# Performance work log

Measured on AMD Instinct MI355X. Metric: run time of the kernel, lower is better.

## Reference

```python
import jax, jax.numpy as jnp
import numpy as np

N_NODES = 50000
N_EDGES = 400000
N_GRAPHS = 16
IN_DIM_NODE = 6
IN_DIM_EDGE = 2
HIDDEN = 64
N_LAYERS = 3
STATE_DIM = 4
MLP1, MLP2 = 256, 256
MAX_ACTION = 1.0
BN_EPS = 1e-5


def _lin(key, fan_in, fan_out):
    k1, k2 = jax.random.split(key)
    s = 1.0 / np.sqrt(fan_in)
    w = jax.random.uniform(k1, (fan_in, fan_out), minval=-s, maxval=s, dtype=jnp.float32)
    b = jax.random.uniform(k2, (fan_out,), minval=-s, maxval=s, dtype=jnp.float32)
    return w, b


def setup_inputs() -> dict:
    key = jax.random.key(0)
    ks = jax.random.split(key, 32)
    inp = {}
    inp["state"] = jax.random.normal(ks[0], (N_GRAPHS, STATE_DIM), dtype=jnp.float32)
    inp["h_feat"] = jax.random.normal(ks[1], (N_NODES, IN_DIM_NODE), dtype=jnp.float32)
    # positive edge features (distances) bounded away from 0 since forward takes 1/e
    inp["e_feat"] = jax.random.uniform(ks[2], (N_EDGES, IN_DIM_EDGE), minval=0.5, maxval=1.5, dtype=jnp.float32)
    inp["src"] = jax.random.randint(ks[3], (N_EDGES,), 0, N_NODES, dtype=jnp.int32)
    inp["dst"] = jax.random.randint(ks[4], (N_EDGES,), 0, N_NODES, dtype=jnp.int32)
    inp["graph_ids"] = jnp.sort(jax.random.randint(ks[5], (N_NODES,), 0, N_GRAPHS, dtype=jnp.int32))
    inp["emb_h_w"], inp["emb_h_b"] = _lin(ks[6], IN_DIM_NODE, HIDDEN)
    inp["emb_e_w"], inp["emb_e_b"] = _lin(ks[7], IN_DIM_EDGE, HIDDEN)
    for i, name in enumerate(["A", "B", "C", "D", "E"]):
        ws, bs = [], []
        for l in range(N_LAYERS):
            w, b = _lin(jax.random.fold_in(ks[8 + i], l), HIDDEN, HIDDEN)
            ws.append(w); bs.append(b)
        inp[name + "_w"] = jnp.stack(ws)  # [L, H, H]
        inp[name + "_b"] = jnp.stack(bs)  # [L, H]
    inp["bn_h_g"] = jnp.ones((N_LAYERS, HIDDEN), jnp.float32)
    inp["bn_h_b"] = jnp.zeros((N_LAYERS, HIDDEN), jnp.float32)
    inp["bn_e_g"] = jnp.ones((N_LAYERS, HIDDEN), jnp.float32)
    inp["bn_e_b"] = jnp.zeros((N_LAYERS, HIDDEN), jnp.float32)
    inp["l1_w"], inp["l1_b"] = _lin(ks[13], HIDDEN + STATE_DIM, MLP1)
    inp["l2_w"], inp["l2_b"] = _lin(ks[14], MLP1, MLP2)
    inp["l3_w"], inp["l3_b"] = _lin(ks[15], MLP2, 2)
    return inp


def _bn(x, g, b):
    mu = jnp.mean(x, axis=0)
    var = jnp.var(x, axis=0)
    return (x - mu) * jax.lax.rsqrt(var + BN_EPS) * g + b


def reference(state, h_feat, e_feat, src, dst, graph_ids,
              emb_h_w, emb_h_b, emb_e_w, emb_e_b,
              A_w, A_b, B_w, B_b, C_w, C_b, D_w, D_b, E_w, E_b,
              bn_h_g, bn_h_b, bn_e_g, bn_e_b,
              l1_w, l1_b, l2_w, l2_b, l3_w, l3_b):
    N = h_feat.shape[0]
    B = state.shape[0]
    # feature prep: concat node states, reciprocal edge states
    e = 1.0 / e_feat
    h = h_feat @ emb_h_w + emb_h_b          # [N, H]
    e = e @ emb_e_w + emb_e_b               # [E, H]
    for l in range(N_LAYERS):
        h_in, e_in = h, e
        Ah = h @ A_w[l] + A_b[l]
        Bh = h @ B_w[l] + B_b[l]
        Dh = h @ D_w[l] + D_b[l]
        Eh = h @ E_w[l] + E_b[l]
        Ce = e @ C_w[l] + C_b[l]
        e_hat = Dh[src] + Eh[dst] + Ce      # [E, H] edge gates pre-activation
        sigma = jax.nn.sigmoid(e_hat)
        num = jax.ops.segment_sum(sigma * Bh[src], dst, num_segments=N)
        den = jax.ops.segment_sum(sigma, dst, num_segments=N)
        h_new = Ah + num / (den + 1e-6)
        h = h_in + jax.nn.relu(_bn(h_new, bn_h_g[l], bn_h_b[l]))
        e = e_in + jax.nn.relu(_bn(e_hat, bn_e_g[l], bn_e_b[l]))
    # mean readout per graph
    counts = jax.ops.segment_sum(jnp.ones((N,), h.dtype), graph_ids, num_segments=B)
    hg = jax.ops.segment_sum(h, graph_ids, num_segments=B) / counts[:, None]
    x = jnp.concatenate([hg, state], axis=-1)
    x = jax.nn.relu(x @ l1_w + l1_b)
    x = jax.nn.relu(x @ l2_w + l2_b)
    return MAX_ACTION * jnp.tanh(x @ l3_w + l3_b)
```

## Files before the change

kernel.cpp:

```cpp
#include <hip/hip_runtime.h>
#include <hip/hip_fp16.h>
#include <math.h>
#include <string.h>

#define NN 50000
#define NE 400000

__device__ __forceinline__ void atomAddF(float* p, float v) { unsafeAtomicAdd(p, v); }
__device__ __forceinline__ double atomAddD(double* p, double v) { return unsafeAtomicAdd(p, v); }
__device__ __forceinline__ int atomAddI(int* p, int v) { return atomicAdd(p, v); }

typedef _Float16 h2v __attribute__((ext_vector_type(2)));

__device__ __forceinline__ float2 up2h(unsigned v) {
  __half2 h; memcpy(&h, &v, 4); return __half22float2(h);
}
__device__ __forceinline__ unsigned pk2h(float a, float b) {
  __half2 h = __floats2half2_rn(a, b);
  unsigned v; memcpy(&v, &h, 4); return v;
}
__device__ __forceinline__ void up8(uint4 u, float* f) {
  float2 a = up2h(u.x), b = up2h(u.y), c = up2h(u.z), d = up2h(u.w);
  f[0] = a.x; f[1] = a.y; f[2] = b.x; f[3] = b.y;
  f[4] = c.x; f[5] = c.y; f[6] = d.x; f[7] = d.y;
}
__device__ __forceinline__ uint4 pk8(const float* f) {
  uint4 u;
  u.x = pk2h(f[0], f[1]); u.y = pk2h(f[2], f[3]);
  u.z = pk2h(f[4], f[5]); u.w = pk2h(f[6], f[7]);
  return u;
}

#if __has_builtin(__builtin_amdgcn_fdot2)
__device__ __forceinline__ float dot2(unsigned a, unsigned b, float c) {
  return __builtin_amdgcn_fdot2(__builtin_bit_cast(h2v, a), __builtin_bit_cast(h2v, b), c, false);
}
#else
__device__ __forceinline__ float dot2(unsigned a, unsigned b, float c) {
  float2 fa = up2h(a), fb = up2h(b);
  return c + fa.x * fb.x + fa.y * fb.y;
}
#endif

#define SW(kk) ((((kk) & 7)) << 2)

__global__ __launch_bounds__(256) void k_zero(float4* __restrict__ p, int n4) {
  int i = blockIdx.x * 256 + threadIdx.x;
  int s = gridDim.x * 256;
  for (; i < n4; i += s) p[i] = make_float4(0.f, 0.f, 0.f, 0.f);
}

__global__ __launch_bounds__(256) void k_deg(const int* __restrict__ dst, int* __restrict__ deg) {
  int i = blockIdx.x * 256 + threadIdx.x;
  if (i < NE) atomAddI(&deg[dst[i]], 1);
}

__global__ __launch_bounds__(1024) void k_scan(int* __restrict__ degcur,
    int* __restrict__ offs, double* __restrict__ stats) {
  __shared__ int wsum[16];
  int t = threadIdx.x;
  int lane = t & 63, w = t >> 6;
  if (t < 256) stats[t] = 0.0;
  int carry = 0;
  for (int base = 0; base < NN; base += 1024) {
    int i = base + t;
    int v = (i < NN) ? degcur[i] : 0;
    int x = v;
    #pragma unroll
    for (int off = 1; off < 64; off <<= 1) {
      int y = __shfl_up(x, off);
      if (lane >= off) x += y;
    }
    if (lane == 63) wsum[w] = x;
    __syncthreads();
    if (w == 0 && lane < 16) {
      int s = wsum[lane];
      #pragma unroll
      for (int off = 1; off < 16; off <<= 1) {
        int y = __shfl_up(s, off);
        if (lane >= off) s += y;
      }
      wsum[lane] = s;
    }
    __syncthreads();
    int wbase = (w > 0) ? wsum[w - 1] : 0;
    int total = wsum[15];
    int excl = carry + wbase + x - v;
    if (i < NN) { offs[i] = excl; degcur[i] = excl; }
    carry += total;
    __syncthreads();
  }
  if (t == 0) offs[NN] = carry;
}

__global__ __launch_bounds__(256) void k_scatter(const int* __restrict__ dst,
    const int* __restrict__ src, const float* __restrict__ e_feat,
    int* __restrict__ cursor,
    int* __restrict__ srcp, int* __restrict__ dstp, float* __restrict__ ef2) {
  int i = blockIdx.x * 256 + threadIdx.x;
  if (i < NE) {
    int d = dst[i];
    int p = atomAddI(&cursor[d], 1);
    srcp[p] = src[i];
    dstp[p] = d;
    ((float2*)ef2)[p] = ((const float2*)e_feat)[i];
  }
}

template <int MODE>
__global__ __launch_bounds__(512) void k_node_gemm(float* __restrict__ h,
    const __half* __restrict__ Ah_in, const float* __restrict__ bnp,
    const float* __restrict__ hf, const float* __restrict__ ehw,
    const float* __restrict__ ehb,
    const float* __restrict__ w0, const float* __restrict__ w1,
    const float* __restrict__ w2, const float* __restrict__ w3,
    const float* __restrict__ b0, const float* __restrict__ b1,
    const float* __restrict__ b2, const float* __restrict__ b3,
    __half* __restrict__ Ah16, __half* __restrict__ Bh16,
    __half* __restrict__ Dh16, __half* __restrict__ Eh16) {
  __shared__ __align__(16) unsigned hsU[32 * 256];
  __shared__ __align__(16) unsigned wshU[32 * 64];
  int t = threadIdx.x;
  int n0 = blockIdx.x * 256;
  #pragma unroll
  for (int i = 0; i < 8; ++i) {
    int f = (t + i * 512) * 4;
    int r = f >> 6;
    int k = f & 63;
    int n = n0 + r;
    float4 v = make_float4(0.f, 0.f, 0.f, 0.f);
    if (n < NN) {
      size_t idx = (size_t)n * 64 + k;
      if (MODE == 2) {
        const float* row = hf + (size_t)n * 6;
        v = *(const float4*)(ehb + k);
        #pragma unroll
        for (int q = 0; q < 6; ++q) {
          float x = row[q];
          float4 wv = *(const float4*)(ehw + q * 64 + k);
          v.x += x * wv.x; v.y += x * wv.y; v.z += x * wv.z; v.w += x * wv.w;
        }
        *(float4*)(h + idx) = v;
      } else {
        v = *(const float4*)(h + idx);
        if (MODE == 1) {
          uint2 au = *(const uint2*)(Ah_in + idx);
          float2 a01 = up2h(au.x), a23 = up2h(au.y);
          float4 sc4 = *(const float4*)(bnp + k);
          float4 sh4 = *(const float4*)(bnp + 64 + k);
          v.x += fmaxf(a01.x * sc4.x + sh4.x, 0.f);
          v.y += fmaxf(a01.y * sc4.y + sh4.y, 0.f);
          v.z += fmaxf(a23.x * sc4.z + sh4.z, 0.f);
          v.w += fmaxf(a23.y * sc4.w + sh4.w, 0.f);
          *(float4*)(h + idx) = v;
        }
      }
    }
    int kk0 = k >> 1;
    hsU[(kk0 + 0) * 256 + (r ^ SW(kk0 + 0))] = pk2h(v.x, v.y);
    hsU[(kk0 + 1) * 256 + (r ^ SW(kk0 + 1))] = pk2h(v.z, v.w);
  }
  int cg = t & 7, rg = t >> 3;
  int cb = cg * 8;
  #pragma unroll 1
  for (int y = 0; y < 4; ++y) {
    const float* W = (y == 0) ? w0 : (y == 1) ? w1 : (y == 2) ? w2 : w3;
    const float* B = (y == 0) ? b0 : (y == 1) ? b1 : (y == 2) ? b2 : b3;
    __syncthreads();
    #pragma unroll
    for (int i = 0; i < 4; ++i) {
      int idx = t + i * 512;
      int kk = idx >> 6, j = idx & 63;
      wshU[idx] = pk2h(W[(2 * kk) * 64 + j], W[(2 * kk + 1) * 64 + j]);
    }
    __syncthreads();
    float acc[4][8];
    #pragma unroll
    for (int r = 0; r < 4; ++r)
      #pragma unroll
      for (int j = 0; j < 8; ++j) acc[r][j] = 0.f;
    #pragma unroll 8
    for (int kk = 0; kk < 32; ++kk) {
      uint4 a4 = *(const uint4*)&hsU[kk * 256 + ((rg * 4) ^ SW(kk))];
      uint4 wA = *(const uint4*)&wshU[kk * 64 + cb];
      uint4 wB = *(const uint4*)&wshU[kk * 64 + cb + 4];
      unsigned av[4] = {a4.x, a4.y, a4.z, a4.w};
      unsigned wv[8] = {wA.x, wA.y, wA.z, wA.w, wB.x, wB.y, wB.z, wB.w};
      #pragma unroll
      for (int r = 0; r < 4; ++r)
        #pragma unroll
        for (int j = 0; j < 8; ++j) acc[r][j] = dot2(av[r], wv[j], acc[r][j]);
    }
    float4 bv0 = *(const float4*)(B + cb);
    float4 bv1 = *(const float4*)(B + cb + 4);
    float bv[8] = {bv0.x, bv0.y, bv0.z, bv0.w, bv1.x, bv1.y, bv1.z, bv1.w};
    __half* oh = (y == 0) ? Ah16 : (y == 1) ? Bh16 : (y == 2) ? Dh16 : Eh16;
    #pragma unroll
    for (int r = 0; r < 4; ++r) {
      int n = n0 + rg * 4 + r;
      if (n < NN) {
        float o[8];
        #pragma unroll
        for (int j = 0; j < 8; ++j) o[j] = acc[r][j] + bv[j];
        *(uint4*)(oh + (size_t)n * 64 + cb) = pk8(o);
      }
    }
  }
}

template <int MODE, int ESTATS, int EWRITE>
__global__ __launch_bounds__(512) void k_edge_f(__half* __restrict__ e16,
    __half* __restrict__ eh16,
    const float* __restrict__ Cw, const float* __restrict__ Cb,
    const int* __restrict__ srcp, const int* __restrict__ dstp,
    const __half* __restrict__ Dh16, const __half* __restrict__ Eh16,
    const float* __restrict__ bnp, double* __restrict__ stats,
    const float* __restrict__ ef2, const float* __restrict__ ew,
    const float* __restrict__ eb) {
  __shared__ __align__(16) unsigned esU[32 * 256];
  __shared__ __align__(16) unsigned cwU[32 * 64];
  int t = threadIdx.x;
  int e0 = blockIdx.x * 256;
  #pragma unroll
  for (int i = 0; i < 4; ++i) {
    int idx = t + i * 512;
    int kk = idx >> 6, j = idx & 63;
    cwU[idx] = pk2h(Cw[(2 * kk) * 64 + j], Cw[(2 * kk + 1) * 64 + j]);
  }
  #pragma unroll
  for (int i = 0; i < 4; ++i) {
    int f = (t + i * 512) * 8;
    int r = f >> 6;
    int k = f & 63;
    int row = e0 + r;
    uint4 raw = make_uint4(0u, 0u, 0u, 0u);
    if (row < NE) {
      size_t idx = (size_t)row * 64 + k;
      if (MODE == 2) {
        float2 rp = ((const float2*)ef2)[row];
        float r0 = 1.0f / rp.x;
        float r1 = 1.0f / rp.y;
        float4 bA = *(const float4*)(eb + k), bB = *(const float4*)(eb + k + 4);
        float4 waA = *(const float4*)(ew + k), waB = *(const float4*)(ew + k + 4);
        float4 wbA = *(const float4*)(ew + 64 + k), wbB = *(const float4*)(ew + 64 + k + 4);
        float v[8];
        v[0] = bA.x + r0 * waA.x + r1 * wbA.x;
        v[1] = bA.y + r0 * waA.y + r1 * wbA.y;
        v[2] = bA.z + r0 * waA.z + r1 * wbA.z;
        v[3] = bA.w + r0 * waA.w + r1 * wbA.w;
        v[4] = bB.x + r0 * waB.x + r1 * wbB.x;
        v[5] = bB.y + r0 * waB.y + r1 * wbB.y;
        v[6] = bB.z + r0 * waB.z + r1 * wbB.z;
        v[7] = bB.w + r0 * waB.w + r1 * wbB.w;
        raw = pk8(v);
        if (EWRITE) *(uint4*)(e16 + idx) = raw;
      } else {
        raw = *(const uint4*)(e16 + idx);
        if (MODE == 1) {
          float v[8], pp[8];
          up8(raw, v);
          up8(*(const uint4*)(eh16 + idx), pp);
          float4 scA = *(const float4*)(bnp + 128 + k);
          float4 scB = *(const float4*)(bnp + 128 + k + 4);
          float4 shA = *(const float4*)(bnp + 192 + k);
          float4 shB = *(const float4*)(bnp + 192 + k + 4);
          float sc[8] = {scA.x, scA.y, scA.z, scA.w, scB.x, scB.y, scB.z, scB.w};
          float sh[8] = {shA.x, shA.y, shA.z, shA.w, shB.x, shB.y, shB.z, shB.w};
          #pragma unroll
          for (int j = 0; j < 8; ++j) v[j] += fmaxf(pp[j] * sc[j] + sh[j], 0.f);
          raw = pk8(v);
          if (EWRITE) *(uint4*)(e16 + idx) = raw;
        }
      }
    }
    int kk0 = k >> 1;
    esU[(kk0 + 0) * 256 + (r ^ SW(kk0 + 0))] = raw.x;
    esU[(kk0 + 1) * 256 + (r ^ SW(kk0 + 1))] = raw.y;
    esU[(kk0 + 2) * 256 + (r ^ SW(kk0 + 2))] = raw.z;
    esU[(kk0 + 3) * 256 + (r ^ SW(kk0 + 3))] = raw.w;
  }
  __syncthreads();
  int cg = t & 7, rg = t >> 3;
  int cb = cg * 8;
  float acc[4][8];
  #pragma unroll
  for (int r = 0; r < 4; ++r)
    #pragma unroll
    for (int j = 0; j < 8; ++j) acc[r][j] = 0.f;
  #pragma unroll 8
  for (int kk = 0; kk < 32; ++kk) {
    uint4 a4 = *(const uint4*)&esU[kk * 256 + ((rg * 4) ^ SW(kk))];
    uint4 wA = *(const uint4*)&cwU[kk * 64 + cb];
    uint4 wB = *(const uint4*)&cwU[kk * 64 + cb + 4];
    unsigned av[4] = {a4.x, a4.y, a4.z, a4.w};
    unsigned wv[8] = {wA.x, wA.y, wA.z, wA.w, wB.x, wB.y, wB.z, wB.w};
    #pragma unroll
    for (int r = 0; r < 4; ++r)
      #pragma unroll
      for (int j = 0; j < 8; ++j) acc[r][j] = dot2(av[r], wv[j], acc[r][j]);
  }
  float4 cb0 = *(const float4*)(Cb + cb);
  float4 cb1 = *(const float4*)(Cb + cb + 4);
  float cbv[8] = {cb0.x, cb0.y, cb0.z, cb0.w, cb1.x, cb1.y, cb1.z, cb1.w};
  float psum[8], psq[8];
  #pragma unroll
  for (int j = 0; j < 8; ++j) { psum[j] = 0.f; psq[j] = 0.f; }
  #pragma unroll
  for (int r = 0; r < 4; ++r) {
    int p = e0 + rg * 4 + r;
    if (p < NE) {
      int sN = srcp[p], dN = dstp[p];
      float dd[8], qq[8];
      up8(*(const uint4*)(Dh16 + (size_t)sN * 64 + cb), dd);
      up8(*(const uint4*)(Eh16 + (size_t)dN * 64 + cb), qq);
      float ev[8];
      #pragma unroll
      for (int j = 0; j < 8; ++j) {
        float v = acc[r][j] + cbv[j] + dd[j] + qq[j];
        ev[j] = v;
        if (ESTATS) { psum[j] += v; psq[j] += v * v; }
      }
      *(uint4*)(eh16 + (size_t)p * 64 + cb) = pk8(ev);
    }
  }
  if (ESTATS) {
    float* red = (float*)esU;
    __syncthreads();
    #pragma unroll
    for (int j = 0; j < 8; ++j) red[rg * 65 + cb + j] = psum[j];
    __syncthreads();
    if (t < 64) {
      float s = 0.f;
      #pragma unroll
      for (int i = 0; i < 64; ++i) s += red[i * 65 + t];
      atomAddD(stats + 128 + t, (double)s);
    }
    __syncthreads();
    #pragma unroll
    for (int j = 0; j < 8; ++j) red[rg * 65 + cb + j] = psq[j];
    __syncthreads();
    if (t < 64) {
      float q = 0.f;
      #pragma unroll
      for (int i = 0; i < 64; ++i) q += red[i * 65 + t];
      atomAddD(stats + 192 + t, (double)q);
    }
  }
}

template <int LAST>
__global__ __launch_bounds__(1024) void k_agg(const int* __restrict__ offs,
    const int* __restrict__ srcp, const __half* __restrict__ eh16,
    const __half* __restrict__ Bh16, __half* __restrict__ Ah16, double* __restrict__ stats,
    int* __restrict__ ctr,
    const float* __restrict__ hgam, const float* __restrict__ hbet,
    const float* __restrict__ egam, const float* __restrict__ ebet,
    float* __restrict__ bnp, float* __restrict__ hg) {
  int t = threadIdx.x;
  int c = t & 63;
  int g = t >> 6;
  float psum = 0.f, psq = 0.f;
  #pragma unroll 1
  for (int sub = 0; sub < 8; ++sub) {
    int n = blockIdx.x * 128 + g * 8 + sub;
    if (n < NN) {
      int i0 = offs[n], i1 = offs[n + 1];
      float num = 0.f, den = 0.f;
      int i = i0;
      #pragma unroll 1
      for (; i + 3 < i1; i += 4) {
        float x0 = __half2float(eh16[(size_t)(i + 0) * 64 + c]);
        float x1 = __half2float(eh16[(size_t)(i + 1) * 64 + c]);
        float x2 = __half2float(eh16[(size_t)(i + 2) * 64 + c]);
        float x3 = __half2float(eh16[(size_t)(i + 3) * 64 + c]);
        int s0 = srcp[i], s1 = srcp[i + 1], s2 = srcp[i + 2], s3 = srcp[i + 3];
        float b0 = __half2float(Bh16[(size_t)s0 * 64 + c]);
        float b1 = __half2float(Bh16[(size_t)s1 * 64 + c]);
        float b2 = __half2float(Bh16[(size_t)s2 * 64 + c]);
        float b3 = __half2float(Bh16[(size_t)s3 * 64 + c]);
        float g0 = 1.0f / (1.0f + __expf(-x0));
        float g1 = 1.0f / (1.0f + __expf(-x1));
        float g2 = 1.0f / (1.0f + __expf(-x2));
        float g3 = 1.0f / (1.0f + __expf(-x3));
        num += g0 * b0 + g1 * b1 + g2 * b2 + g3 * b3;
        den += g0 + g1 + g2 + g3;
      }
      #pragma unroll 1
      for (; i < i1; ++i) {
        float x0 = __half2float(eh16[(size_t)i * 64 + c]);
        int s0 = srcp[i];
        float b0 = __half2float(Bh16[(size_t)s0 * 64 + c]);
        float g0 = 1.0f / (1.0f + __expf(-x0));
        num += g0 * b0;
        den += g0;
      }
      size_t idx = (size_t)n * 64 + c;
      float v = __half2float(Ah16[idx]) + num / (den + 1e-6f);
      Ah16[idx] = __float2half(v);
      psum += v; psq += v * v;
    }
  }
  __shared__ float red[1024];
  red[t] = psum; __syncthreads();
  if (t < 64) {
    float s = 0.f;
    #pragma unroll
    for (int i = 0; i < 16; ++i) s += red[t + i * 64];
    atomAddD(stats + t, (double)s);
  }
  __syncthreads();
  red[t] = psq; __syncthreads();
  if (t < 64) {
    float q = 0.f;
    #pragma unroll
    for (int i = 0; i < 16; ++i) q += red[t + i * 64];
    atomAddD(stats + 64 + t, (double)q);
  }
  __shared__ int lastFlag;
  __syncthreads();
  if (t == 0) {
    __threadfence();
    int old = atomAddI(ctr, 1);
    lastFlag = (old == (int)gridDim.x - 1);
  }
  __syncthreads();
  if (!lastFlag) return;
  if (t < 64) {
    double s = atomAddD(stats + t, 0.0);
    double q = atomAddD(stats + 64 + t, 0.0);
    double mu = s * (1.0 / NN);
    double var = q * (1.0 / NN) - mu * mu;
    float sc = hgam[t] / sqrtf((float)var + 1e-5f);
    bnp[t] = sc;
    bnp[64 + t] = hbet[t] - (float)mu * sc;
  } else if (t < 128) {
    int cc = t - 64;
    double s = atomAddD(stats + 128 + cc, 0.0);
    double q = atomAddD(stats + 192 + cc, 0.0);
    double mu = s * (1.0 / NE);
    double var = q * (1.0 / NE) - mu * mu;
    float sc = egam[cc] / sqrtf((float)var + 1e-5f);
    bnp[128 + cc] = sc;
    bnp[192 + cc] = ebet[cc] - (float)mu * sc;
  }
  __syncthreads();
  if (t < 256) atomicExch((unsigned long long*)&stats[t], 0ull);
  if (LAST) {
    for (int i = t; i < 1040; i += 1024) hg[i] = 0.f;
  }
}

__global__ __launch_bounds__(256) void k_readout(const float* __restrict__ h,
    const __half* __restrict__ Ah16, const float* __restrict__ bnp,
    const int* __restrict__ gid, float* __restrict__ hg, float* __restrict__ counts) {
  int t = threadIdx.x;
  int c = t & 63;
  int ro = t >> 6;
  int nbase = blockIdx.x * 256;
  float sc = bnp[c], sh = bnp[64 + c];
  float sum = 0.f, cnt = 0.f;
  int curg = -1;
  #pragma unroll 1
  for (int i = 0; i < 64; ++i) {
    int n = nbase + ro + i * 4;
    if (n >= NN) break;
    int g = gid[n];
    if (g != curg) {
      if (curg >= 0) {
        atomAddF(&hg[curg * 64 + c], sum);
        if (c == 0) atomAddF(&counts[curg], cnt);
      }
      curg = g; sum = 0.f; cnt = 0.f;
    }
    size_t idx = (size_t)n * 64 + c;
    float av = __half2float(Ah16[idx]);
    sum += h[idx] + fmaxf(av * sc + sh, 0.f);
    cnt += 1.f;
  }
  if (curg >= 0) {
    atomAddF(&hg[curg * 64 + c], sum);
    if (c == 0) atomAddF(&counts[curg], cnt);
  }
}

__global__ __launch_bounds__(256) void k_mlp(const float* __restrict__ hg, const float* __restrict__ counts,
    const float* __restrict__ state,
    const float* __restrict__ w1, const float* __restrict__ b1,
    const float* __restrict__ w2, const float* __restrict__ b2,
    const float* __restrict__ w3, const float* __restrict__ b3,
    float* __restrict__ out) {
  __shared__ float x0[16][68];
  __shared__ float x1[16][256];
  __shared__ float x2[16][256];
  int t = threadIdx.x;
  for (int idx = t; idx < 16 * 68; idx += 256) {
    int g = idx / 68, c = idx % 68;
    x0[g][c] = (c < 64) ? hg[g * 64 + c] / counts[g] : state[g * 4 + (c - 64)];
  }
  __syncthreads();
  {
    float acc[16];
    float bb = b1[t];
    #pragma unroll
    for (int g = 0; g < 16; ++g) acc[g] = bb;
    for (int k = 0; k < 68; ++k) {
      float w = w1[k * 256 + t];
      #pragma unroll
      for (int g = 0; g < 16; ++g) acc[g] += x0[g][k] * w;
    }
    #pragma unroll
    for (int g = 0; g < 16; ++g) x1[g][t] = fmaxf(acc[g], 0.f);
  }
  __syncthreads();
  {
    float acc[16];
    float bb = b2[t];
    #pragma unroll
    for (int g = 0; g < 16; ++g) acc[g] = bb;
    for (int k = 0; k < 256; ++k) {
      float w = w2[k * 256 + t];
      #pragma unroll
      for (int g = 0; g < 16; ++g) acc[g] += x1[g][k] * w;
    }
    #pragma unroll
    for (int g = 0; g < 16; ++g) x2[g][t] = fmaxf(acc[g], 0.f);
  }
  __syncthreads();
  if (t < 32) {
    int g = t >> 1, o = t & 1;
    float acc = b3[o];
    for (int k = 0; k < 256; ++k) acc += x2[g][k] * w3[k * 2 + o];
    out[g * 2 + o] = tanhf(acc);
  }
}

extern "C" void kernel_launch(void* const* d_in, const int* in_sizes, int n_in,
                              void* d_out, int out_size, void* d_ws, size_t ws_size,
                              hipStream_t stream) {
  const float* state   = (const float*)d_in[0];
  const float* h_feat  = (const float*)d_in[1];
  const float* e_feat  = (const float*)d_in[2];
  const int*   src     = (const int*)d_in[3];
  const int*   dst     = (const int*)d_in[4];
  const int*   gid     = (const int*)d_in[5];
  const float* emb_h_w = (const float*)d_in[6];
  const float* emb_h_b = (const float*)d_in[7];
  const float* emb_e_w = (const float*)d_in[8];
  const float* emb_e_b = (const float*)d_in[9];
  const float* A_w = (const float*)d_in[10];
  const float* A_b = (const float*)d_in[11];
  const float* B_w = (const float*)d_in[12];
  const float* B_b = (const float*)d_in[13];
  const float* C_w = (const float*)d_in[14];
  const float* C_b = (const float*)d_in[15];
  const float* D_w = (const float*)d_in[16];
  const float* D_b = (const float*)d_in[17];
  const float* E_w = (const float*)d_in[18];
  const float* E_b = (const float*)d_in[19];
  const float* bn_h_g = (const float*)d_in[20];
  const float* bn_h_b = (const float*)d_in[21];
  const float* bn_e_g = (const float*)d_in[22];
  const float* bn_e_b = (const float*)d_in[23];
  const float* l1_w = (const float*)d_in[24];
  const float* l1_b = (const float*)d_in[25];
  const float* l2_w = (const float*)d_in[26];
  const float* l2_b = (const float*)d_in[27];
  const float* l3_w = (const float*)d_in[28];
  const float* l3_b = (const float*)d_in[29];

  float* wsp = (float*)d_ws;

  const size_t F_H = (size_t)NN * 64;
  const size_t F_H2 = (size_t)NN * 32;
  const size_t F_E2 = (size_t)NE * 32;
  size_t off = 0;
  float*  h     = wsp + off; off += F_H;
  __half* Ah16  = (__half*)(wsp + off); off += F_H2;
  __half* e16   = (__half*)(wsp + off); off += F_E2;
  __half* eh16  = (__half*)(wsp + off); off += F_E2;
  float*  ef2   = wsp + off; off += (size_t)NE * 2;
  __half* Bh16  = (__half*)(wsp + off); off += F_H2;
  __half* Dh16  = (__half*)(wsp + off); off += F_H2;
  __half* Eh16  = (__half*)(wsp + off); off += F_H2;
  int* srcp    = (int*)(wsp + off); off += NE;
  int* dstp    = (int*)(wsp + off); off += NE;
  int* offs    = (int*)(wsp + off); off += NN + 4;
  int* degcur  = (int*)(wsp + off); off += NN + 4;
  double* stats = (double*)(wsp + off); off += 512;
  float* bnp    = wsp + off; off += 256;
  float* hg     = wsp + off; off += 1024;
  float* counts = hg + 1024; off += 16;
  const size_t need = off * sizeof(float);
  if (ws_size < need) return;
  int* ctr = degcur + NN;

  k_zero<<<64, 256, 0, stream>>>((float4*)degcur, (NN + 4) / 4);
  k_deg<<<(NE + 255) / 256, 256, 0, stream>>>(dst, degcur);
  k_scan<<<1, 1024, 0, stream>>>(degcur, offs, stats);
  k_scatter<<<(NE + 255) / 256, 256, 0, stream>>>(dst, src, e_feat, degcur, srcp, dstp, ef2);

  const int GN = (NN + 255) / 256;
  const int GE = (NE + 255) / 256;
  const int GA = (NN + 127) / 128;
  for (int l = 0; l < 3; ++l) {
    if (l == 0)
      k_node_gemm<2><<<GN, 512, 0, stream>>>(h, Ah16, bnp, h_feat, emb_h_w, emb_h_b,
          A_w, B_w, D_w, E_w, A_b, B_b, D_b, E_b, Ah16, Bh16, Dh16, Eh16);
    else
      k_node_gemm<1><<<GN, 512, 0, stream>>>(h, Ah16, bnp, h_feat, emb_h_w, emb_h_b,
          A_w + l * 4096, B_w + l * 4096, D_w + l * 4096, E_w + l * 4096,
          A_b + l * 64, B_b + l * 64, D_b + l * 64, E_b + l * 64,
          Ah16, Bh16, Dh16, Eh16);
    if (l == 0)
      k_edge_f<2, 1, 1><<<GE, 512, 0, stream>>>(e16, eh16, C_w, C_b,
          srcp, dstp, Dh16, Eh16, bnp, stats, ef2, emb_e_w, emb_e_b);
    else if (l == 1)
      k_edge_f<1, 1, 1><<<GE, 512, 0, stream>>>(e16, eh16, C_w + 4096, C_b + 64,
          srcp, dstp, Dh16, Eh16, bnp, stats, ef2, emb_e_w, emb_e_b);
    else
      k_edge_f<1, 0, 0><<<GE, 512, 0, stream>>>(e16, eh16, C_w + 8192, C_b + 128,
          srcp, dstp, Dh16, Eh16, bnp, stats, ef2, emb_e_w, emb_e_b);
    if (l < 2)
      k_agg<0><<<GA, 1024, 0, stream>>>(offs, srcp, eh16, Bh16, Ah16, stats, ctr + l,
          bn_h_g + l * 64, bn_h_b + l * 64, bn_e_g + l * 64, bn_e_b + l * 64, bnp, hg);
    else
      k_agg<1><<<GA, 1024, 0, stream>>>(offs, srcp, eh16, Bh16, Ah16, stats, ctr + l,
          bn_h_g + l * 64, bn_h_b + l * 64, bn_e_g + l * 64, bn_e_b + l * 64, bnp, hg);
  }
  k_readout<<<(NN + 255) / 256, 256, 0, stream>>>(h, Ah16, bnp, gid, hg, counts);
  k_mlp<<<1, 256, 0, stream>>>(hg, counts, state,
      l1_w, l1_b, l2_w, l2_b, l3_w, l3_b, (float*)d_out);
}
```

Measured before the change: 584.2 us.

## Replace single-block degree scan with three-phase multi-block scan

The exclusive prefix sum over node degrees ran in one 1024-thread block that looped serially over about 49 chunks. It is now split into a per-block local scan, a single-block scan of the 196 block sums, and an add-back pass. This spreads the scan across many CUs, at the cost of two extra kernel launches and an extra intermediate array. The final offset is now written as the constant NE instead of the computed total.

```diff
diff --git a/kernel.cpp b/kernel.cpp
--- a/kernel.cpp
+++ b/kernel.cpp
@@ -55,42 +55,58 @@
   if (i < NE) atomAddI(&deg[dst[i]], 1);
 }
 
-__global__ __launch_bounds__(1024) void k_scan(int* __restrict__ degcur,
-    int* __restrict__ offs, double* __restrict__ stats) {
-  __shared__ int wsum[16];
+__global__ __launch_bounds__(256) void k_scanA(const int* __restrict__ deg,
+    int* __restrict__ locx, int* __restrict__ bsum) {
+  __shared__ int wsum[4];
   int t = threadIdx.x;
+  int i = blockIdx.x * 256 + t;
+  int v = (i < NN) ? deg[i] : 0;
   int lane = t & 63, w = t >> 6;
-  if (t < 256) stats[t] = 0.0;
-  int carry = 0;
-  for (int base = 0; base < NN; base += 1024) {
-    int i = base + t;
-    int v = (i < NN) ? degcur[i] : 0;
-    int x = v;
-    #pragma unroll
-    for (int off = 1; off < 64; off <<= 1) {
-      int y = __shfl_up(x, off);
-      if (lane >= off) x += y;
-    }
-    if (lane == 63) wsum[w] = x;
-    __syncthreads();
-    if (w == 0 && lane < 16) {
-      int s = wsum[lane];
-      #pragma unroll
-      for (int off = 1; off < 16; off <<= 1) {
-        int y = __shfl_up(s, off);
-        if (lane >= off) s += y;
-      }
-      wsum[lane] = s;
-    }
-    __syncthreads();
-    int wbase = (w > 0) ? wsum[w - 1] : 0;
-    int total = wsum[15];
-    int excl = carry + wbase + x - v;
-    if (i < NN) { offs[i] = excl; degcur[i] = excl; }
-    carry += total;
-    __syncthreads();
-  }
-  if (t == 0) offs[NN] = carry;
+  int x = v;
+  #pragma unroll
+  for (int off = 1; off < 64; off <<= 1) {
+    int y = __shfl_up(x, off);
+    if (lane >= off) x += y;
+  }
+  if (lane == 63) wsum[w] = x;
+  __syncthreads();
+  int wbase = 0;
+  #pragma unroll
+  for (int j = 0; j < 4; ++j) if (j < w) wbase += wsum[j];
+  if (i < NN) locx[i] = wbase + x - v;
+  if (t == 255) bsum[blockIdx.x] = wbase + x;
+}
+
+__global__ __launch_bounds__(256) void k_scanB(int* __restrict__ bsum, int nb,
+    double* __restrict__ stats) {
+  __shared__ int wsum[4];
+  int t = threadIdx.x;
+  stats[t] = 0.0;
+  int v = (t < nb) ? bsum[t] : 0;
+  int lane = t & 63, w = t >> 6;
+  int x = v;
+  #pragma unroll
+  for (int off = 1; off < 64; off <<= 1) {
+    int y = __shfl_up(x, off);
+    if (lane >= off) x += y;
+  }
+  if (lane == 63) wsum[w] = x;
+  __syncthreads();
+  int wbase = 0;
+  #pragma unroll
+  for (int j = 0; j < 4; ++j) if (j < w) wbase += wsum[j];
+  if (t < nb) bsum[t] = wbase + x - v;
+}
+
+__global__ __launch_bounds__(256) void k_scanC(const int* __restrict__ locx,
+    const int* __restrict__ bsum, int* __restrict__ offs, int* __restrict__ cursor) {
+  int i = blockIdx.x * 256 + threadIdx.x;
+  if (i < NN) {
+    int v = locx[i] + bsum[blockIdx.x];
+    offs[i] = v;
+    cursor[i] = v;
+  }
+  if (i == 0) offs[NN] = NE;
 }
 
 __global__ __launch_bounds__(256) void k_scatter(const int* __restrict__ dst,
@@ -586,6 +602,8 @@
   int* dstp    = (int*)(wsp + off); off += NE;
   int* offs    = (int*)(wsp + off); off += NN + 4;
   int* degcur  = (int*)(wsp + off); off += NN + 4;
+  int* locx    = (int*)(wsp + off); off += NN;
+  int* bsum    = (int*)(wsp + off); off += 256;
   double* stats = (double*)(wsp + off); off += 512;
   float* bnp    = wsp + off; off += 256;
   float* hg     = wsp + off; off += 1024;
@@ -594,9 +612,13 @@
   if (ws_size < need) return;
   int* ctr = degcur + NN;
 
+  const int NB = (NN + 255) / 256;
+
   k_zero<<<64, 256, 0, stream>>>((float4*)degcur, (NN + 4) / 4);
   k_deg<<<(NE + 255) / 256, 256, 0, stream>>>(dst, degcur);
-  k_scan<<<1, 1024, 0, stream>>>(degcur, offs, stats);
+  k_scanA<<<NB, 256, 0, stream>>>(degcur, locx, bsum);
+  k_scanB<<<1, 256, 0, stream>>>(bsum, NB, stats);
+  k_scanC<<<NB, 256, 0, stream>>>(locx, bsum, offs, degcur);
   k_scatter<<<(NE + 255) / 256, 256, 0, stream>>>(dst, src, e_feat, degcur, srcp, dstp, ef2);
 
   const int GN = (NN + 255) / 256;
```

Result: faster. 549.2 us (-6.0%).
